# Kernel tuning notes

Hardware: AMD Instinct MI355X
Metric: run time of the kernel (lower is better)

## Reference

```python
import jax, jax.numpy as jnp
import numpy as np

E, H, FF = 1024, 16, 4096
HD = E // H
B, S = 4, 2048


def _ln(x, g, b, eps=1e-5):
    m = jnp.mean(x, axis=-1, keepdims=True)
    v = jnp.mean((x - m) ** 2, axis=-1, keepdims=True)
    return (x - m) / jnp.sqrt(v + eps) * g + b


def setup_inputs() -> dict:
    k = jax.random.key(0)
    ks = jax.random.split(k, 12)
    sd = 0.02
    return {
        "value": jax.random.normal(ks[0], (B, S, E), jnp.float32),
        "key": jax.random.normal(ks[1], (B, S, E), jnp.float32),
        "query": jax.random.normal(ks[2], (B, S, E), jnp.float32),
        "mask": jnp.ones((B, 1, 1, S), jnp.int32),
        "Wv": sd * jax.random.normal(ks[3], (E, E), jnp.float32),
        "Wk": sd * jax.random.normal(ks[4], (E, E), jnp.float32),
        "Wq": sd * jax.random.normal(ks[5], (E, E), jnp.float32),
        "Wo": sd * jax.random.normal(ks[6], (E, E), jnp.float32),
        "bo": jnp.zeros((E,), jnp.float32),
        "ln1_g": jnp.ones((E,), jnp.float32), "ln1_b": jnp.zeros((E,), jnp.float32),
        "ln2_g": jnp.ones((E,), jnp.float32), "ln2_b": jnp.zeros((E,), jnp.float32),
        "lnf_g": jnp.ones((E,), jnp.float32), "lnf_b": jnp.zeros((E,), jnp.float32),
        "W1": sd * jax.random.normal(ks[7], (E, FF), jnp.float32),
        "b1": jnp.zeros((FF,), jnp.float32),
        "W2": sd * jax.random.normal(ks[8], (FF, E), jnp.float32),
        "b2": jnp.zeros((E,), jnp.float32),
    }


def reference(value, key, query, mask, Wv, Wk, Wq, Wo, bo,
              ln1_g, ln1_b, ln2_g, ln2_b, lnf_g, lnf_b, W1, b1, W2, b2):
    N, Sq, Em = query.shape
    # pre-norms (value & key share prenorm2 params, as in the torch module)
    v = _ln(value, ln2_g, ln2_b)
    k = _ln(key, ln2_g, ln2_b)
    q = _ln(query, ln1_g, ln1_b)
    # QKV projections (no bias), split heads
    V = (v @ Wv).reshape(N, v.shape[1], H, HD)
    K = (k @ Wk).reshape(N, k.shape[1], H, HD)
    Q = (q @ Wq).reshape(N, Sq, H, HD)
    energy = jnp.einsum("nqhd,nkhd->nhqk", Q, K)  # [N,H,Sq,Sk]
    energy = jnp.where(mask == 0, jnp.float32(-1e20), energy)
    attn = jax.nn.softmax(energy / jnp.float32(HD ** 0.5), axis=-1)
    out = jnp.einsum("nhqk,nkhd->nqhd", attn, V).reshape(N, Sq, Em)
    out = out @ Wo + bo
    x = out + q  # residual (drop_path is identity in eval)
    f = _ln(x, lnf_g, lnf_b) @ W1 + b1
    f = jax.nn.gelu(f, approximate=False) @ W2 + b2
    return f + x
```

## Files before the change

kernel.cpp:

```cpp
#include <hip/hip_runtime.h>
#include <hip/hip_bf16.h>
#include <math.h>

typedef __bf16 bf16x8 __attribute__((ext_vector_type(8)));
typedef __bf16 bf16x4 __attribute__((ext_vector_type(4)));
typedef float f32x4 __attribute__((ext_vector_type(4)));
typedef float f32x2 __attribute__((ext_vector_type(2)));
typedef short s16x4 __attribute__((ext_vector_type(4)));

#define AS1 __attribute__((address_space(1)))
#define AS3 __attribute__((address_space(3)))

__device__ __forceinline__ void gll16(const __bf16* g, __bf16* l) {
    __builtin_amdgcn_global_load_lds((const AS1 unsigned int*)g,
                                     (AS3 unsigned int*)l, 16, 0, 0);
}

#if __has_builtin(__builtin_amdgcn_exp2f)
#define EXP2(x) __builtin_amdgcn_exp2f(x)
#else
#define EXP2(x) __expf((x) * 0.69314718055994530942f)
#endif

__device__ __forceinline__ f32x4 mfma16x16(bf16x4 a, bf16x4 b, f32x4 c) {
#if __has_builtin(__builtin_amdgcn_mfma_f32_16x16x16bf16_1k)
    union { bf16x4 h; s16x4 s; } ua, ub;
    ua.h = a; ub.h = b;
    return __builtin_amdgcn_mfma_f32_16x16x16bf16_1k(ua.s, ub.s, c, 0, 0, 0);
#else
    f32x4 d = c;
    asm volatile("v_mfma_f32_16x16x16_bf16 %0, %1, %2, %0"
                 : "+v"(d) : "v"(a), "v"(b));
    return d;
#endif
}

__global__ __launch_bounds__(256) void transpose_all(
    const float* __restrict__ Wq, const float* __restrict__ Wk,
    const float* __restrict__ Wv, const float* __restrict__ Wo,
    const float* __restrict__ W1, const float* __restrict__ W2,
    __bf16* __restrict__ Wqt, __bf16* __restrict__ Wkt,
    __bf16* __restrict__ Wvt, __bf16* __restrict__ Wot,
    __bf16* __restrict__ W1t, __bf16* __restrict__ W2t) {
    int g = blockIdx.x;
    const float* W; __bf16* Wt; int K, N, kt, nt;
    if (g < 4096) {
        int mi = g >> 10, loc = g & 1023;
        K = 1024; N = 1024; kt = loc >> 5; nt = loc & 31;
        W  = mi == 0 ? Wq  : mi == 1 ? Wk  : mi == 2 ? Wv  : Wo;
        Wt = mi == 0 ? Wqt : mi == 1 ? Wkt : mi == 2 ? Wvt : Wot;
    } else if (g < 8192) {
        int loc = g - 4096; W = W1; Wt = W1t;
        K = 1024; N = 4096; kt = loc >> 7; nt = loc & 127;
    } else {
        int loc = g - 8192; W = W2; Wt = W2t;
        K = 4096; N = 1024; kt = loc >> 5; nt = loc & 31;
    }
    int k0 = kt * 32, n0 = nt * 32;
    __shared__ float tile[32][33];
    int tx = threadIdx.x & 31, ty = threadIdx.x >> 5;
    #pragma unroll
    for (int j = ty; j < 32; j += 8)
        tile[j][tx] = W[(size_t)(k0 + j) * N + n0 + tx];
    __syncthreads();
    #pragma unroll
    for (int j = ty; j < 32; j += 8)
        Wt[(size_t)(n0 + j) * K + k0 + tx] = (__bf16)tile[tx][j];
}

__global__ __launch_bounds__(256) void ln3_kernel(
    const float* __restrict__ q, const float* __restrict__ k,
    const float* __restrict__ v,
    const float* __restrict__ g1, const float* __restrict__ b1,
    const float* __restrict__ g2, const float* __restrict__ b2,
    float* __restrict__ qln, __bf16* __restrict__ qbf,
    __bf16* __restrict__ kbf, __bf16* __restrict__ vbf) {
    const int E = 1024;
    int which = blockIdx.y;
    const float* x = which == 0 ? q : which == 1 ? k : v;
    const float* g = which == 0 ? g1 : g2;
    const float* bb = which == 0 ? b1 : b2;
    float* o32 = which == 0 ? qln : nullptr;
    __bf16* obf = which == 0 ? qbf : which == 1 ? kbf : vbf;

    size_t row = blockIdx.x;
    int t = threadIdx.x;
    float4 val = ((const float4*)(x + row * E))[t];
    float s  = val.x + val.y + val.z + val.w;
    float s2 = val.x * val.x + val.y * val.y + val.z * val.z + val.w * val.w;
    #pragma unroll
    for (int off = 32; off >= 1; off >>= 1) {
        s  += __shfl_down(s, off);
        s2 += __shfl_down(s2, off);
    }
    __shared__ float red[2][4];
    int wid = t >> 6, lane = t & 63;
    if (lane == 0) { red[0][wid] = s; red[1][wid] = s2; }
    __syncthreads();
    if (t == 0) {
        float S1 = red[0][0] + red[0][1] + red[0][2] + red[0][3];
        float S2 = red[1][0] + red[1][1] + red[1][2] + red[1][3];
        float mean = S1 / E;
        float var  = S2 / E - mean * mean;
        red[0][0] = mean;
        red[1][0] = 1.0f / sqrtf(var + 1e-5f);
    }
    __syncthreads();
    float mean = red[0][0], rstd = red[1][0];
    float4 gv = ((const float4*)g)[t];
    float4 bv = ((const float4*)bb)[t];
    float y0 = (val.x - mean) * rstd * gv.x + bv.x;
    float y1 = (val.y - mean) * rstd * gv.y + bv.y;
    float y2 = (val.z - mean) * rstd * gv.z + bv.z;
    float y3 = (val.w - mean) * rstd * gv.w + bv.w;
    if (o32) ((float4*)(o32 + row * E))[t] = make_float4(y0, y1, y2, y3);
    bf16x4 o;
    o[0] = (__bf16)y0; o[1] = (__bf16)y1; o[2] = (__bf16)y2; o[3] = (__bf16)y3;
    ((bf16x4*)(obf + row * E))[t] = o;
}

__global__ __launch_bounds__(256) void ln_kernel(const float* __restrict__ x,
                                                 const float* __restrict__ g,
                                                 const float* __restrict__ bb,
                                                 __bf16* __restrict__ outbf) {
    const int E = 1024;
    size_t row = blockIdx.x;
    int t = threadIdx.x;
    float4 v = ((const float4*)(x + row * E))[t];
    float s  = v.x + v.y + v.z + v.w;
    float s2 = v.x * v.x + v.y * v.y + v.z * v.z + v.w * v.w;
    #pragma unroll
    for (int off = 32; off >= 1; off >>= 1) {
        s  += __shfl_down(s, off);
        s2 += __shfl_down(s2, off);
    }
    __shared__ float red[2][4];
    int wid = t >> 6, lane = t & 63;
    if (lane == 0) { red[0][wid] = s; red[1][wid] = s2; }
    __syncthreads();
    if (t == 0) {
        float S1 = red[0][0] + red[0][1] + red[0][2] + red[0][3];
        float S2 = red[1][0] + red[1][1] + red[1][2] + red[1][3];
        float mean = S1 / E;
        float var  = S2 / E - mean * mean;
        red[0][0] = mean;
        red[1][0] = 1.0f / sqrtf(var + 1e-5f);
    }
    __syncthreads();
    float mean = red[0][0], rstd = red[1][0];
    float4 gv = ((const float4*)g)[t];
    float4 bv = ((const float4*)bb)[t];
    bf16x4 o;
    o[0] = (__bf16)((v.x - mean) * rstd * gv.x + bv.x);
    o[1] = (__bf16)((v.y - mean) * rstd * gv.y + bv.y);
    o[2] = (__bf16)((v.z - mean) * rstd * gv.z + bv.z);
    o[3] = (__bf16)((v.w - mean) * rstd * gv.w + bv.w);
    ((bf16x4*)(outbf + row * E))[t] = o;
}

template <int EPI>
__global__ __launch_bounds__(256) void gemm128(const __bf16* __restrict__ A,
                                               const __bf16* __restrict__ A2,
                                               const __bf16* __restrict__ Bt,
                                               const __bf16* __restrict__ Bt2,
                                               const float* __restrict__ bias,
                                               const float* __restrict__ resid,
                                               void* __restrict__ Cout,
                                               int M, int N, int K,
                                               int splitN, float scale) {
    __shared__ __bf16 As[128 * 64];
    __shared__ __bf16 Bs[128 * 64];
    int tid  = threadIdx.x;
    int lane = tid & 63, wid = tid >> 6;
    int quad = lane >> 4, l15 = lane & 15;
    int waveM = wid >> 1, waveN = wid & 1;

    int GX = N >> 7;
    int id = blockIdx.x;
    int x8 = id & 7, t = id >> 3;
    size_t rowBase = (size_t)((t / GX) * 8 + x8) * 128;
    size_t colBase = (size_t)(t % GX) * 128;

    const __bf16* Ap = A; const __bf16* Bp = Bt;
    size_t colLoc = colBase;
    float sc = scale;
    if ((int)colBase >= splitN) { Ap = A2; Bp = Bt2; colLoc = colBase - splitN; sc = 1.0f; }

    int lrow8  = lane >> 3;
    int lchunk = (lane & 7) ^ lrow8;
    const __bf16* Ag0 = Ap + (rowBase + wid * 32 + lrow8) * (size_t)K + lchunk * 8;
    const __bf16* Bg0 = Bp + (colLoc  + wid * 32 + lrow8) * (size_t)K + lchunk * 8;
    __bf16* AsB = &As[(wid * 32) * 64];
    __bf16* BsB = &Bs[(wid * 32) * 64];

    f32x4 acc[4][4] = {};
    int swz = l15 & 7;

    for (int kb = 0; kb < K; kb += 64) {
        __syncthreads();
        #pragma unroll
        for (int i = 0; i < 4; i++) {
            gll16(Ag0 + (size_t)i * 8 * K + kb, AsB + i * 512);
            gll16(Bg0 + (size_t)i * 8 * K + kb, BsB + i * 512);
        }
        __syncthreads();
        #pragma unroll
        for (int ks = 0; ks < 2; ks++) {
            int p = ((ks * 4 + quad) ^ swz) * 8;
            bf16x8 af[4], bfr[4];
            #pragma unroll
            for (int mi = 0; mi < 4; mi++)
                af[mi] = *(const bf16x8*)&As[(waveM * 64 + mi * 16 + l15) * 64 + p];
            #pragma unroll
            for (int ni = 0; ni < 4; ni++)
                bfr[ni] = *(const bf16x8*)&Bs[(waveN * 64 + ni * 16 + l15) * 64 + p];
            #pragma unroll
            for (int mi = 0; mi < 4; mi++)
                #pragma unroll
                for (int ni = 0; ni < 4; ni++)
                    acc[mi][ni] = __builtin_amdgcn_mfma_f32_16x16x32_bf16(
                        bfr[ni], af[mi], acc[mi][ni], 0, 0, 0);
        }
    }

    #pragma unroll
    for (int mi = 0; mi < 4; mi++)
    #pragma unroll
    for (int ni = 0; ni < 4; ni++) {
        size_t row = rowBase + waveM * 64 + mi * 16 + l15;
        size_t col = colBase + waveN * 64 + ni * 16 + quad * 4;
        f32x4 v = acc[mi][ni];
        if (EPI == 1) {
            float4 b4 = *(const float4*)&bias[col];
            float4 r4 = *(const float4*)&resid[row * N + col];
            float4 o;
            o.x = v[0] + b4.x + r4.x; o.y = v[1] + b4.y + r4.y;
            o.z = v[2] + b4.z + r4.z; o.w = v[3] + b4.w + r4.w;
            *(float4*)&((float*)Cout)[row * N + col] = o;
        } else if (EPI == 2) {
            float4 b4 = *(const float4*)&bias[col];
            bf16x4 pk;
            #pragma unroll
            for (int r = 0; r < 4; r++) {
                float t2 = v[r] + ((const float*)&b4)[r];
                pk[r] = (__bf16)(0.5f * t2 * (1.0f + erff(t2 * 0.70710678118654752f)));
            }
            *(bf16x4*)&((__bf16*)Cout)[row * N + col] = pk;
        } else {
            bf16x4 pk;
            #pragma unroll
            for (int r = 0; r < 4; r++) pk[r] = (__bf16)(v[r] * sc);
            *(bf16x4*)&((__bf16*)Cout)[row * N + col] = pk;
        }
    }
}

__global__ __launch_bounds__(256) void gemmV(const __bf16* __restrict__ A,
                                             const __bf16* __restrict__ Bt,
                                             __bf16* __restrict__ Cout,
                                             int M, int N, int K) {
    __shared__ __bf16 As[128 * 64];
    __shared__ __bf16 Bs[128 * 64];
    int tid  = threadIdx.x;
    int lane = tid & 63, wid = tid >> 6;
    int quad = lane >> 4, l15 = lane & 15;
    int waveM = wid >> 1, waveN = wid & 1;

    int GX = N >> 7;
    int id = blockIdx.x;
    int x8 = id & 7, t = id >> 3;
    size_t rowBase = (size_t)((t / GX) * 8 + x8) * 128;
    size_t colBase = (size_t)(t % GX) * 128;

    int lrow8  = lane >> 3;
    int lchunk = (lane & 7) ^ lrow8;
    const __bf16* Ag0 = A  + (rowBase + wid * 32 + lrow8) * (size_t)K + lchunk * 8;
    const __bf16* Bg0 = Bt + (colBase + wid * 32 + lrow8) * (size_t)K + lchunk * 8;
    __bf16* AsB = &As[(wid * 32) * 64];
    __bf16* BsB = &Bs[(wid * 32) * 64];

    f32x4 acc[4][4] = {};
    int swz = l15 & 7;

    for (int kb = 0; kb < K; kb += 64) {
        __syncthreads();
        #pragma unroll
        for (int i = 0; i < 4; i++) {
            gll16(Ag0 + (size_t)i * 8 * K + kb, AsB + i * 512);
            gll16(Bg0 + (size_t)i * 8 * K + kb, BsB + i * 512);
        }
        __syncthreads();
        #pragma unroll
        for (int ks = 0; ks < 2; ks++) {
            int p = ((ks * 4 + quad) ^ swz) * 8;
            bf16x8 af[4], bfr[4];
            #pragma unroll
            for (int mi = 0; mi < 4; mi++)
                af[mi] = *(const bf16x8*)&As[(waveM * 64 + mi * 16 + l15) * 64 + p];
            #pragma unroll
            for (int ni = 0; ni < 4; ni++)
                bfr[ni] = *(const bf16x8*)&Bs[(waveN * 64 + ni * 16 + l15) * 64 + p];
            #pragma unroll
            for (int mi = 0; mi < 4; mi++)
                #pragma unroll
                for (int ni = 0; ni < 4; ni++)
                    acc[mi][ni] = __builtin_amdgcn_mfma_f32_16x16x32_bf16(
                        af[mi], bfr[ni], acc[mi][ni], 0, 0, 0);
        }
    }

    #pragma unroll
    for (int mi = 0; mi < 4; mi++)
    #pragma unroll
    for (int ni = 0; ni < 4; ni++) {
        size_t col = colBase + waveN * 64 + ni * 16 + l15;
        size_t m0  = rowBase + waveM * 64 + mi * 16 + quad * 4;
        bf16x4 pk;
        #pragma unroll
        for (int r = 0; r < 4; r++) pk[r] = (__bf16)acc[mi][ni][r];
        *(bf16x4*)&Cout[col * M + m0] = pk;
    }
}

__global__ __launch_bounds__(512, 6) void attn_kernel(const __bf16* __restrict__ QK,
                                                      const __bf16* __restrict__ Vt,
                                                      const int* __restrict__ mask,
                                                      __bf16* __restrict__ Out) {
    const int S = 2048, E = 1024, E2 = 2048, M = 8192;
    int qt = blockIdx.x, bh = blockIdx.y;
    int b = bh >> 4, h = bh & 15;
    int q0 = qt * 128;
    int tid = threadIdx.x, lane = tid & 63, wid = tid >> 6;
    int quad = lane >> 4, l15 = lane & 15;

    __shared__ __bf16 Ks[2][4096];
    __shared__ __bf16 Vs[2][4096];

    bf16x8 aq[2];
    #pragma unroll
    for (int hh = 0; hh < 2; hh++) {
        size_t row = (size_t)(b * S + q0 + wid * 16 + l15);
        aq[hh] = *(const bf16x8*)(QK + row * E2 + h * 64 + hh * 32 + quad * 8);
    }

    int lrow8  = lane >> 3;
    int lchunk = (lane & 7) ^ lrow8;
    const __bf16* Kg0 = QK + (size_t)(b * S + wid * 8 + lrow8) * E2 + 1024 + h * 64 + lchunk * 8;

    int rv = tid >> 3, cv = tid & 7;
    const __bf16* Vg0 = Vt + (size_t)(h * 64 + rv) * M + b * S + cv * 8;
    int c0   = ((cv & 1) << 2) + (cv >> 2);
    int lowb = (cv >> 1) & 1;
    int sv   = rv & 7;
    int wo0  = rv * 64 + ((c0 ^ sv) << 3) + (lowb << 2);
    int wo1  = rv * 64 + ((((c0 + 2)) ^ sv) << 3) + (lowb << 2);

    int swz = l15 & 7;

    f32x4 accO[4] = {};
    f32x2 acc2 = {0.f, 0.f};

    bf16x8 vreg = *(const bf16x8*)(Vg0);
    gll16(Kg0, &Ks[0][wid * 512]);
    {
        *(bf16x4*)&Vs[0][wo0] = __builtin_shufflevector(vreg, vreg, 0, 1, 2, 3);
        *(bf16x4*)&Vs[0][wo1] = __builtin_shufflevector(vreg, vreg, 4, 5, 6, 7);
    }
    __syncthreads();

    for (int kt = 0; kt < S / 64; kt++) {
        int k0 = kt * 64;
        int buf = kt & 1;
        if (kt + 1 < S / 64) {
            vreg = *(const bf16x8*)(Vg0 + k0 + 64);
            gll16(Kg0 + (size_t)(k0 + 64) * E2, &Ks[buf ^ 1][wid * 512]);
        }
        const __bf16* Ksb = &Ks[buf][0];
        const __bf16* Vsb = &Vs[buf][0];

        f32x4 sa[4];
        #pragma unroll
        for (int nt = 0; nt < 4; nt++) {
            bf16x8 a0 = *(const bf16x8*)&Ksb[(nt * 16 + l15) * 64 + ((quad) ^ swz) * 8];
            bf16x8 a1 = *(const bf16x8*)&Ksb[(nt * 16 + l15) * 64 + ((4 + quad) ^ swz) * 8];
            f32x4 a = {};
            a = __builtin_amdgcn_mfma_f32_16x16x32_bf16(a0, aq[0], a, 0, 0, 0);
            a = __builtin_amdgcn_mfma_f32_16x16x32_bf16(a1, aq[1], a, 0, 0, 0);
            sa[nt] = a;
        }

        bf16x4 pb[4];
        #pragma unroll
        for (int nt = 0; nt < 4; nt++) {
            int4 mz = *(const int4*)&mask[b * S + k0 + nt * 16 + quad * 4];
            float p0 = mz.x ? EXP2(sa[nt][0]) : 0.f;
            float p1 = mz.y ? EXP2(sa[nt][1]) : 0.f;
            float p2 = mz.z ? EXP2(sa[nt][2]) : 0.f;
            float p3 = mz.w ? EXP2(sa[nt][3]) : 0.f;
            f32x2 t01; t01[0] = p0; t01[1] = p1;
            f32x2 t23; t23[0] = p2; t23[1] = p3;
            acc2 += t01 + t23;
            bf16x4 pk;
            pk[0] = (__bf16)p0; pk[1] = (__bf16)p1;
            pk[2] = (__bf16)p2; pk[3] = (__bf16)p3;
            pb[nt] = pk;
        }

        #pragma unroll
        for (int dt = 0; dt < 4; dt++) {
            const __bf16* vrow = &Vsb[(dt * 16 + l15) * 64];
            bf16x8 vv0 = *(const bf16x8*)&vrow[((quad * 2 + 0) ^ swz) * 8];
            bf16x8 vv1 = *(const bf16x8*)&vrow[((quad * 2 + 1) ^ swz) * 8];
            accO[dt] = mfma16x16(__builtin_shufflevector(vv0, vv0, 0, 1, 2, 3), pb[0], accO[dt]);
            accO[dt] = mfma16x16(__builtin_shufflevector(vv0, vv0, 4, 5, 6, 7), pb[1], accO[dt]);
            accO[dt] = mfma16x16(__builtin_shufflevector(vv1, vv1, 0, 1, 2, 3), pb[2], accO[dt]);
            accO[dt] = mfma16x16(__builtin_shufflevector(vv1, vv1, 4, 5, 6, 7), pb[3], accO[dt]);
        }

        if (kt + 1 < S / 64) {
            *(bf16x4*)&Vs[buf ^ 1][wo0] = __builtin_shufflevector(vreg, vreg, 0, 1, 2, 3);
            *(bf16x4*)&Vs[buf ^ 1][wo1] = __builtin_shufflevector(vreg, vreg, 4, 5, 6, 7);
        }
        __syncthreads();
    }

    float l = acc2[0] + acc2[1];
    l += __shfl_xor(l, 16, 64);
    l += __shfl_xor(l, 32, 64);
    float inv = 1.0f / l;

    #pragma unroll
    for (int dt = 0; dt < 4; dt++) {
        size_t row = (size_t)(b * S + q0 + wid * 16 + l15);
        bf16x4 pk;
        #pragma unroll
        for (int r = 0; r < 4; r++) pk[r] = (__bf16)(accO[dt][r] * inv);
        *(bf16x4*)&Out[row * E + h * 64 + dt * 16 + quad * 4] = pk;
    }
}

extern "C" void kernel_launch(void* const* d_in, const int* in_sizes, int n_in,
                              void* d_out, int out_size, void* d_ws, size_t ws_size,
                              hipStream_t stream) {
    const int Bb = 4, S = 2048, E = 1024, FF = 4096;
    const int M = Bb * S;

    const float* value = (const float*)d_in[0];
    const float* key   = (const float*)d_in[1];
    const float* query = (const float*)d_in[2];
    const int*   mask  = (const int*)d_in[3];
    const float* Wv    = (const float*)d_in[4];
    const float* Wk    = (const float*)d_in[5];
    const float* Wq    = (const float*)d_in[6];
    const float* Wo    = (const float*)d_in[7];
    const float* bo    = (const float*)d_in[8];
    const float* ln1_g = (const float*)d_in[9];
    const float* ln1_b = (const float*)d_in[10];
    const float* ln2_g = (const float*)d_in[11];
    const float* ln2_b = (const float*)d_in[12];
    const float* lnf_g = (const float*)d_in[13];
    const float* lnf_b = (const float*)d_in[14];
    const float* W1    = (const float*)d_in[15];
    const float* b1    = (const float*)d_in[16];
    const float* W2    = (const float*)d_in[17];
    const float* b2    = (const float*)d_in[18];

    char* ws = (char*)d_ws;
    const size_t MB = 1024 * 1024;
    __bf16* Wqt = (__bf16*)(ws + 0 * MB);
    __bf16* Wkt = (__bf16*)(ws + 2 * MB);
    __bf16* Wvt = (__bf16*)(ws + 4 * MB);
    __bf16* Wot = (__bf16*)(ws + 6 * MB);
    __bf16* W1t = (__bf16*)(ws + 8 * MB);
    __bf16* W2t = (__bf16*)(ws + 16 * MB);
    __bf16* q_bf = (__bf16*)(ws + 24 * MB);
    __bf16* k_bf = (__bf16*)(ws + 40 * MB);
    __bf16* v_bf = (__bf16*)(ws + 56 * MB);
    __bf16* QKb  = (__bf16*)(ws + 72 * MB);
    __bf16* Vtg  = (__bf16*)(ws + 104 * MB);
    __bf16* attn = q_bf;
    __bf16* x_ln = k_bf;
    __bf16* h1   = v_bf;
    float*  qln  = (float*)(ws + 120 * MB);
    float*  x32  = (float*)(ws + 152 * MB);

    transpose_all<<<12288, 256, 0, stream>>>(Wq, Wk, Wv, Wo, W1, W2,
                                             Wqt, Wkt, Wvt, Wot, W1t, W2t);

    ln3_kernel<<<dim3(M, 3), 256, 0, stream>>>(query, key, value,
                                               ln1_g, ln1_b, ln2_g, ln2_b,
                                               qln, q_bf, k_bf, v_bf);

    gemm128<0><<<16 * 64, 256, 0, stream>>>(
        q_bf, k_bf, Wqt, Wkt, nullptr, nullptr, QKb, M, 2 * E, E, E,
        0.125f * 1.44269504088896f);

    gemmV<<<8 * 64, 256, 0, stream>>>(v_bf, Wvt, Vtg, M, E, E);

    attn_kernel<<<dim3(S / 128, Bb * 16), 512, 0, stream>>>(QKb, Vtg, mask, attn);

    gemm128<1><<<8 * 64, 256, 0, stream>>>(
        attn, attn, Wot, Wot, bo, qln, x32, M, E, E, E, 1.0f);

    ln_kernel<<<M, 256, 0, stream>>>(x32, lnf_g, lnf_b, x_ln);

    gemm128<2><<<32 * 64, 256, 0, stream>>>(
        x_ln, x_ln, W1t, W1t, b1, nullptr, h1, M, FF, E, FF, 1.0f);
    gemm128<1><<<8 * 64, 256, 0, stream>>>(
        h1, h1, W2t, W2t, b2, x32, (float*)d_out, M, E, FF, E, 1.0f);
}
```

Measured before the change: 669.2 us.

## Process two query row groups per wave in attention to reuse K/V tiles

Each wave now computes attention for 32 query rows (two 16-row groups) instead of 16, doubling the block's query tile to 256 and halving the grid. K and V tiles staged in LDS are reused across both groups, cutting global/LDS load traffic per unit of MFMA work. It raises register pressure (launch bounds lowered from 6 to 4 blocks) and halves the number of blocks, which may reduce latency hiding.

```diff
diff --git a/kernel.cpp b/kernel.cpp
--- a/kernel.cpp
+++ b/kernel.cpp
@@ -322,25 +322,27 @@
     }
 }
 
-__global__ __launch_bounds__(512, 6) void attn_kernel(const __bf16* __restrict__ QK,
+__global__ __launch_bounds__(512, 4) void attn_kernel(const __bf16* __restrict__ QK,
                                                       const __bf16* __restrict__ Vt,
                                                       const int* __restrict__ mask,
                                                       __bf16* __restrict__ Out) {
     const int S = 2048, E = 1024, E2 = 2048, M = 8192;
     int qt = blockIdx.x, bh = blockIdx.y;
     int b = bh >> 4, h = bh & 15;
-    int q0 = qt * 128;
+    int q0 = qt * 256;
     int tid = threadIdx.x, lane = tid & 63, wid = tid >> 6;
     int quad = lane >> 4, l15 = lane & 15;
 
     __shared__ __bf16 Ks[2][4096];
     __shared__ __bf16 Vs[2][4096];
 
-    bf16x8 aq[2];
+    bf16x8 aq[2][2];
+    #pragma unroll
+    for (int g = 0; g < 2; g++)
     #pragma unroll
     for (int hh = 0; hh < 2; hh++) {
-        size_t row = (size_t)(b * S + q0 + wid * 16 + l15);
-        aq[hh] = *(const bf16x8*)(QK + row * E2 + h * 64 + hh * 32 + quad * 8);
+        size_t row = (size_t)(b * S + q0 + wid * 32 + g * 16 + l15);
+        aq[g][hh] = *(const bf16x8*)(QK + row * E2 + h * 64 + hh * 32 + quad * 8);
     }
 
     int lrow8  = lane >> 3;
@@ -353,19 +355,17 @@
     int lowb = (cv >> 1) & 1;
     int sv   = rv & 7;
     int wo0  = rv * 64 + ((c0 ^ sv) << 3) + (lowb << 2);
-    int wo1  = rv * 64 + ((((c0 + 2)) ^ sv) << 3) + (lowb << 2);
+    int wo1  = rv * 64 + (((c0 + 2) ^ sv) << 3) + (lowb << 2);
 
     int swz = l15 & 7;
 
-    f32x4 accO[4] = {};
-    f32x2 acc2 = {0.f, 0.f};
+    f32x4 accO[2][4] = {};
+    f32x2 acc2[2] = {};
 
     bf16x8 vreg = *(const bf16x8*)(Vg0);
     gll16(Kg0, &Ks[0][wid * 512]);
-    {
-        *(bf16x4*)&Vs[0][wo0] = __builtin_shufflevector(vreg, vreg, 0, 1, 2, 3);
-        *(bf16x4*)&Vs[0][wo1] = __builtin_shufflevector(vreg, vreg, 4, 5, 6, 7);
-    }
+    *(bf16x4*)&Vs[0][wo0] = __builtin_shufflevector(vreg, vreg, 0, 1, 2, 3);
+    *(bf16x4*)&Vs[0][wo1] = __builtin_shufflevector(vreg, vreg, 4, 5, 6, 7);
     __syncthreads();
 
     for (int kt = 0; kt < S / 64; kt++) {
@@ -378,32 +378,29 @@
         const __bf16* Ksb = &Ks[buf][0];
         const __bf16* Vsb = &Vs[buf][0];
 
-        f32x4 sa[4];
+        bf16x4 pb[2][4];
         #pragma unroll
         for (int nt = 0; nt < 4; nt++) {
             bf16x8 a0 = *(const bf16x8*)&Ksb[(nt * 16 + l15) * 64 + ((quad) ^ swz) * 8];
             bf16x8 a1 = *(const bf16x8*)&Ksb[(nt * 16 + l15) * 64 + ((4 + quad) ^ swz) * 8];
-            f32x4 a = {};
-            a = __builtin_amdgcn_mfma_f32_16x16x32_bf16(a0, aq[0], a, 0, 0, 0);
-            a = __builtin_amdgcn_mfma_f32_16x16x32_bf16(a1, aq[1], a, 0, 0, 0);
-            sa[nt] = a;
-        }
-
-        bf16x4 pb[4];
-        #pragma unroll
-        for (int nt = 0; nt < 4; nt++) {
             int4 mz = *(const int4*)&mask[b * S + k0 + nt * 16 + quad * 4];
-            float p0 = mz.x ? EXP2(sa[nt][0]) : 0.f;
-            float p1 = mz.y ? EXP2(sa[nt][1]) : 0.f;
-            float p2 = mz.z ? EXP2(sa[nt][2]) : 0.f;
-            float p3 = mz.w ? EXP2(sa[nt][3]) : 0.f;
-            f32x2 t01; t01[0] = p0; t01[1] = p1;
-            f32x2 t23; t23[0] = p2; t23[1] = p3;
-            acc2 += t01 + t23;
-            bf16x4 pk;
-            pk[0] = (__bf16)p0; pk[1] = (__bf16)p1;
-            pk[2] = (__bf16)p2; pk[3] = (__bf16)p3;
-            pb[nt] = pk;
+            #pragma unroll
+            for (int g = 0; g < 2; g++) {
+                f32x4 a = {};
+                a = __builtin_amdgcn_mfma_f32_16x16x32_bf16(a0, aq[g][0], a, 0, 0, 0);
+                a = __builtin_amdgcn_mfma_f32_16x16x32_bf16(a1, aq[g][1], a, 0, 0, 0);
+                float p0 = mz.x ? EXP2(a[0]) : 0.f;
+                float p1 = mz.y ? EXP2(a[1]) : 0.f;
+                float p2 = mz.z ? EXP2(a[2]) : 0.f;
+                float p3 = mz.w ? EXP2(a[3]) : 0.f;
+                f32x2 t01; t01[0] = p0; t01[1] = p1;
+                f32x2 t23; t23[0] = p2; t23[1] = p3;
+                acc2[g] += t01 + t23;
+                bf16x4 pk;
+                pk[0] = (__bf16)p0; pk[1] = (__bf16)p1;
+                pk[2] = (__bf16)p2; pk[3] = (__bf16)p3;
+                pb[g][nt] = pk;
+            }
         }
 
         #pragma unroll
@@ -411,10 +408,17 @@
             const __bf16* vrow = &Vsb[(dt * 16 + l15) * 64];
             bf16x8 vv0 = *(const bf16x8*)&vrow[((quad * 2 + 0) ^ swz) * 8];
             bf16x8 vv1 = *(const bf16x8*)&vrow[((quad * 2 + 1) ^ swz) * 8];
-            accO[dt] = mfma16x16(__builtin_shufflevector(vv0, vv0, 0, 1, 2, 3), pb[0], accO[dt]);
-            accO[dt] = mfma16x16(__builtin_shufflevector(vv0, vv0, 4, 5, 6, 7), pb[1], accO[dt]);
-            accO[dt] = mfma16x16(__builtin_shufflevector(vv1, vv1, 0, 1, 2, 3), pb[2], accO[dt]);
-            accO[dt] = mfma16x16(__builtin_shufflevector(vv1, vv1, 4, 5, 6, 7), pb[3], accO[dt]);
+            bf16x4 h00 = __builtin_shufflevector(vv0, vv0, 0, 1, 2, 3);
+            bf16x4 h01 = __builtin_shufflevector(vv0, vv0, 4, 5, 6, 7);
+            bf16x4 h10 = __builtin_shufflevector(vv1, vv1, 0, 1, 2, 3);
+            bf16x4 h11 = __builtin_shufflevector(vv1, vv1, 4, 5, 6, 7);
+            #pragma unroll
+            for (int g = 0; g < 2; g++) {
+                accO[g][dt] = mfma16x16(h00, pb[g][0], accO[g][dt]);
+                accO[g][dt] = mfma16x16(h01, pb[g][1], accO[g][dt]);
+                accO[g][dt] = mfma16x16(h10, pb[g][2], accO[g][dt]);
+                accO[g][dt] = mfma16x16(h11, pb[g][3], accO[g][dt]);
+            }
         }
 
         if (kt + 1 < S / 64) {
@@ -424,18 +428,20 @@
         __syncthreads();
     }
 
-    float l = acc2[0] + acc2[1];
-    l += __shfl_xor(l, 16, 64);
-    l += __shfl_xor(l, 32, 64);
-    float inv = 1.0f / l;
-
-    #pragma unroll
-    for (int dt = 0; dt < 4; dt++) {
-        size_t row = (size_t)(b * S + q0 + wid * 16 + l15);
-        bf16x4 pk;
-        #pragma unroll
-        for (int r = 0; r < 4; r++) pk[r] = (__bf16)(accO[dt][r] * inv);
-        *(bf16x4*)&Out[row * E + h * 64 + dt * 16 + quad * 4] = pk;
+    #pragma unroll
+    for (int g = 0; g < 2; g++) {
+        float l = acc2[g][0] + acc2[g][1];
+        l += __shfl_xor(l, 16, 64);
+        l += __shfl_xor(l, 32, 64);
+        float inv = 1.0f / l;
+        #pragma unroll
+        for (int dt = 0; dt < 4; dt++) {
+            size_t row = (size_t)(b * S + q0 + wid * 32 + g * 16 + l15);
+            bf16x4 pk;
+            #pragma unroll
+            for (int r = 0; r < 4; r++) pk[r] = (__bf16)(accO[g][dt][r] * inv);
+            *(bf16x4*)&Out[row * E + h * 64 + dt * 16 + quad * 4] = pk;
+        }
     }
 }
 
@@ -497,7 +503,7 @@
 
     gemmV<<<8 * 64, 256, 0, stream>>>(v_bf, Wvt, Vtg, M, E, E);
 
-    attn_kernel<<<dim3(S / 128, Bb * 16), 512, 0, stream>>>(QKb, Vtg, mask, attn);
+    attn_kernel<<<dim3(S / 256, Bb * 16), 512, 0, stream>>>(QKb, Vtg, mask, attn);
 
     gemm128<1><<<8 * 64, 256, 0, stream>>>(
         attn, attn, Wot, Wot, bo, qln, x32, M, E, E, E, 1.0f);
```

New measurement: 652.9 us. 1.02x faster.
